# Kernel optimization log

Measured on AMD Instinct MI355X. Metric: run time of the kernel, lower is better.

## Reference

```python
import jax, jax.numpy as jnp
import numpy as np

B, C, H, W, O = 8, 128, 256, 256, 128


def setup_inputs() -> dict:
    key = jax.random.key(0)
    k1, k2, k3, k4 = jax.random.split(key, 4)
    x = jax.random.normal(k1, (B, C, H, W), dtype=jnp.float32)
    theta_s = jax.random.uniform(k2, (C, 2), dtype=jnp.float32, minval=-1.0, maxval=1.0)
    w_dw = jax.random.normal(k3, (C,), dtype=jnp.float32) * 0.1   # depthwise 1x1, groups=C
    w_pw = jax.random.normal(k4, (O, C), dtype=jnp.float32) * (1.0 / np.sqrt(C))  # pointwise 1x1
    return {"x": x, "theta_s": theta_s, "w_dw": w_dw, "w_pw": w_pw}


def reference(x, theta_s, w_dw, w_pw):
    b, c, h, w = x.shape
    # zero pad by 1 (ZeroPad2d(1)); shift operates on the padded map, output is interior
    xp = jnp.pad(x, ((0, 0), (0, 0), (1, 1), (1, 1)))
    hp, wp = h + 2, w + 2
    t = -theta_s                      # (C, 2); torch code negates theta
    ft = jnp.floor(t)
    dt = t - ft                       # fractional part, (C, 2)
    ft = ft.astype(jnp.int32)
    # interior grid of the padded map: rows/cols 1..h / 1..w
    m = jnp.arange(1, h + 1)
    n = jnp.arange(1, w + 1)
    y0 = jnp.clip(m[None, :] + ft[:, 0:1], 0, hp - 1)      # (C, h)
    y1 = jnp.clip(m[None, :] + ft[:, 0:1] + 1, 0, hp - 1)  # (C, h)
    x0 = jnp.clip(n[None, :] + ft[:, 1:2], 0, wp - 1)      # (C, w)
    x1 = jnp.clip(n[None, :] + ft[:, 1:2] + 1, 0, wp - 1)  # (C, w)
    cidx = jnp.arange(c)[:, None, None]                    # (C,1,1)
    # gather four bilinear corners for all channels at once -> (B, C, h, w)
    z1 = xp[:, cidx, y0[:, :, None], x0[:, None, :]]
    z2 = xp[:, cidx, y0[:, :, None], x1[:, None, :]]
    z3 = xp[:, cidx, y1[:, :, None], x0[:, None, :]]
    z4 = xp[:, cidx, y1[:, :, None], x1[:, None, :]]
    dy = dt[:, 0][None, :, None, None]
    dx = dt[:, 1][None, :, None, None]
    s = (z1 * (1 - dy) * (1 - dx) + z2 * (1 - dy) * dx
         + z3 * dy * (1 - dx) + z4 * dy * dx)
    # depthwise 1x1 (groups=C): per-channel scale
    s = s * w_dw[None, :, None, None]
    # pointwise 1x1
    return jnp.einsum('bchw,oc->bohw', s, w_pw)
```

## Files before the change

kernel.cpp:

```cpp
#include <hip/hip_runtime.h>

#define B_ 8
#define C_ 128
#define H_ 256
#define W_ 256
#define O_ 128
#define PAD 136
#define WT 128

typedef __bf16 bf16x4 __attribute__((ext_vector_type(4)));
typedef __bf16 bf16x8 __attribute__((ext_vector_type(8)));
typedef float floatx4 __attribute__((ext_vector_type(4)));

__device__ __forceinline__ float sfloat(float v) {
    return __int_as_float(__builtin_amdgcn_readfirstlane(__float_as_int(v)));
}

__global__ __launch_bounds__(256, 2)
void activeshift_kernel(const float* __restrict__ x,
                        const float* __restrict__ theta,
                        const float* __restrict__ wdw,
                        const float* __restrict__ wpw,
                        float* __restrict__ out)
{
    __shared__ __align__(16) __bf16 w_lds[O_ * PAD];
    __shared__ __align__(16) __bf16 s_lds[WT * PAD];
    __shared__ __align__(16) float  t_q[C_ * 4];
    __shared__ __align__(16) int    t_o[C_ * 4];

    const int bid = blockIdx.x;
    const int n   = ((bid & 7) << 9) | (bid >> 3);
    const int wt  = n & 1;
    const int h   = (n >> 1) & (H_ - 1);
    const int b   = n >> 9;
    const int w0  = wt * WT;
    const int tid = threadIdx.x;
    const int m   = h + 1;

    if (tid < C_) {
        float t0 = -theta[tid * 2 + 0];
        float t1 = -theta[tid * 2 + 1];
        float f0 = floorf(t0), f1 = floorf(t1);
        float dy = t0 - f0,    dx = t1 - f1;
        int ft0 = (int)f0, ft1 = (int)f1;
        int y0 = m + ft0, y1 = y0 + 1;
        float wy0 = (y0 >= 1 && y0 <= H_) ? 1.0f - dy : 0.0f;
        float wy1 = (y1 >= 1 && y1 <= H_) ? dy : 0.0f;
        int y0c = min(max(y0, 1), H_) - 1;
        int y1c = min(max(y1, 1), H_) - 1;
        *(floatx4*)&t_q[tid * 4] = (floatx4){wy0 * (1.0f - dx), wy0 * dx,
                                             wy1 * (1.0f - dx), wy1 * dx};
        *(int4*)&t_o[tid * 4]    = (int4){y0c * W_, y1c * W_, w0 + ft1, 0};
    }

    {
        const int c4 = (tid & 31) << 2;
        const floatx4 dv = *(const floatx4*)&wdw[c4];
        #pragma unroll
        for (int i = 0; i < 16; ++i) {
            int idx4 = tid + i * 256;
            int o    = idx4 >> 5;
            floatx4 v = *(const floatx4*)&wpw[idx4 << 2];
            bf16x4 pk = { (__bf16)(v.x * dv.x), (__bf16)(v.y * dv.y),
                          (__bf16)(v.z * dv.z), (__bf16)(v.w * dv.w) };
            *(bf16x4*)&w_lds[o * PAD + c4] = pk;
        }
    }
    __syncthreads();

    const int p     = tid & (WT - 1);
    const int halfs = __builtin_amdgcn_readfirstlane(tid >> 7);
    const size_t HW = (size_t)H_ * W_;
    const float* xb = x + (size_t)b * C_ * HW;

    for (int it = 0; it < 8; ++it) {
        const int c0 = it * 16 + halfs * 8;
        union { bf16x8 v; __bf16 e[8]; } pk;
        #pragma unroll
        for (int cc = 0; cc < 8; ++cc) {
            const int c = c0 + cc;
            const floatx4 q = *(const floatx4*)&t_q[c * 4];
            const int4   ov = *(const int4*)&t_o[c * 4];
            const float q00 = sfloat(q.x), q01 = sfloat(q.y);
            const float q10 = sfloat(q.z), q11 = sfloat(q.w);
            const int y0off = __builtin_amdgcn_readfirstlane(ov.x);
            const int y1off = __builtin_amdgcn_readfirstlane(ov.y);
            const int xoff  = __builtin_amdgcn_readfirstlane(ov.z);
            const float* r0 = xb + (size_t)c * HW + y0off;
            const float* r1 = xb + (size_t)c * HW + y1off;

            const int ix0 = p + xoff;
            const int vo0 = min(max(ix0, 0), W_ - 1);
            const int vo1 = min(max(ix0 + 1, 0), W_ - 1);
            float v00 = r0[vo0], v01 = r0[vo1];
            float v10 = r1[vo0], v11 = r1[vo1];
            if ((unsigned)ix0       > (unsigned)(W_ - 1)) { v00 = 0.f; v10 = 0.f; }
            if ((unsigned)(ix0 + 1) > (unsigned)(W_ - 1)) { v01 = 0.f; v11 = 0.f; }

            pk.e[cc] = (__bf16)(q00 * v00 + q01 * v01 + q10 * v10 + q11 * v11);
        }
        *(bf16x8*)&s_lds[p * PAD + c0] = pk.v;
    }
    __syncthreads();

    const int wid  = tid >> 6;
    const int lane = tid & 63;
    const int wo   = (wid >> 1) * 64;
    const int wp   = (wid & 1) * 64;
    const int l15  = lane & 15;
    const int quad = lane >> 4;

    floatx4 acc[4][4];
    #pragma unroll
    for (int i = 0; i < 4; ++i)
        #pragma unroll
        for (int j = 0; j < 4; ++j)
            acc[i][j] = (floatx4){0.f, 0.f, 0.f, 0.f};

    #pragma unroll
    for (int k = 0; k < C_; k += 32) {
        bf16x8 af[4], bfr[4];
        #pragma unroll
        for (int i = 0; i < 4; ++i)
            af[i] = *(const bf16x8*)&w_lds[(wo + i * 16 + l15) * PAD + k + quad * 8];
        #pragma unroll
        for (int j = 0; j < 4; ++j)
            bfr[j] = *(const bf16x8*)&s_lds[(wp + j * 16 + l15) * PAD + k + quad * 8];
        #pragma unroll
        for (int i = 0; i < 4; ++i)
            #pragma unroll
            for (int j = 0; j < 4; ++j)
                acc[i][j] = __builtin_amdgcn_mfma_f32_16x16x32_bf16(af[i], bfr[j], acc[i][j], 0, 0, 0);
    }

    float* ob = out + (size_t)b * O_ * HW + (size_t)h * W_;
    #pragma unroll
    for (int i = 0; i < 4; ++i) {
        #pragma unroll
        for (int j = 0; j < 4; ++j) {
            int pcol  = w0 + wp + j * 16 + l15;
            int obase = wo + i * 16 + quad * 4;
            float* op = ob + (size_t)obase * HW + pcol;
            #pragma unroll
            for (int r = 0; r < 4; ++r)
                op[(size_t)r * HW] = acc[i][j][r];
        }
    }
}

extern "C" void kernel_launch(void* const* d_in, const int* in_sizes, int n_in,
                              void* d_out, int out_size, void* d_ws, size_t ws_size,
                              hipStream_t stream) {
    const float* x     = (const float*)d_in[0];
    const float* theta = (const float*)d_in[1];
    const float* wdw   = (const float*)d_in[2];
    const float* wpw   = (const float*)d_in[3];
    float* out = (float*)d_out;
    activeshift_kernel<<<dim3(B_ * H_ * (W_ / WT)), dim3(256), 0, stream>>>(x, theta, wdw, wpw, out);
}
```

Measured before the change: 516.2 us.

## Drop weight LDS staging; load pointwise weights from global in MFMA loop

Removes the per-block staging of the pointwise weight matrix (scaled by depthwise weights) into LDS. The depthwise scale is folded into the bilinear coefficients instead, and the MFMA A-fragments are read straight from global memory and converted to bf16 inside the k loop. Freeing about 34KB of LDS lets launch bounds rise to 4 blocks per CU, aiming for higher occupancy. The cost is repeated global or L2 weight reads and conversions per wave. The readfirstlane scalarization of the coefficients is also dropped.

New measurement: 517.6 us. No clear change (+0.3%).

```diff
diff --git a/kernel.cpp b/kernel.cpp
--- a/kernel.cpp
+++ b/kernel.cpp
@@ -8,22 +8,16 @@
 #define PAD 136
 #define WT 128
 
-typedef __bf16 bf16x4 __attribute__((ext_vector_type(4)));
 typedef __bf16 bf16x8 __attribute__((ext_vector_type(8)));
 typedef float floatx4 __attribute__((ext_vector_type(4)));
 
-__device__ __forceinline__ float sfloat(float v) {
-    return __int_as_float(__builtin_amdgcn_readfirstlane(__float_as_int(v)));
-}
-
-__global__ __launch_bounds__(256, 2)
+__global__ __launch_bounds__(256, 4)
 void activeshift_kernel(const float* __restrict__ x,
                         const float* __restrict__ theta,
                         const float* __restrict__ wdw,
                         const float* __restrict__ wpw,
                         float* __restrict__ out)
 {
-    __shared__ __align__(16) __bf16 w_lds[O_ * PAD];
     __shared__ __align__(16) __bf16 s_lds[WT * PAD];
     __shared__ __align__(16) float  t_q[C_ * 4];
     __shared__ __align__(16) int    t_o[C_ * 4];
@@ -44,27 +38,14 @@
         float dy = t0 - f0,    dx = t1 - f1;
         int ft0 = (int)f0, ft1 = (int)f1;
         int y0 = m + ft0, y1 = y0 + 1;
-        float wy0 = (y0 >= 1 && y0 <= H_) ? 1.0f - dy : 0.0f;
-        float wy1 = (y1 >= 1 && y1 <= H_) ? dy : 0.0f;
+        float dwv = wdw[tid];
+        float wy0 = (y0 >= 1 && y0 <= H_) ? (1.0f - dy) * dwv : 0.0f;
+        float wy1 = (y1 >= 1 && y1 <= H_) ? dy * dwv : 0.0f;
         int y0c = min(max(y0, 1), H_) - 1;
         int y1c = min(max(y1, 1), H_) - 1;
         *(floatx4*)&t_q[tid * 4] = (floatx4){wy0 * (1.0f - dx), wy0 * dx,
                                              wy1 * (1.0f - dx), wy1 * dx};
         *(int4*)&t_o[tid * 4]    = (int4){y0c * W_, y1c * W_, w0 + ft1, 0};
-    }
-
-    {
-        const int c4 = (tid & 31) << 2;
-        const floatx4 dv = *(const floatx4*)&wdw[c4];
-        #pragma unroll
-        for (int i = 0; i < 16; ++i) {
-            int idx4 = tid + i * 256;
-            int o    = idx4 >> 5;
-            floatx4 v = *(const floatx4*)&wpw[idx4 << 2];
-            bf16x4 pk = { (__bf16)(v.x * dv.x), (__bf16)(v.y * dv.y),
-                          (__bf16)(v.z * dv.z), (__bf16)(v.w * dv.w) };
-            *(bf16x4*)&w_lds[o * PAD + c4] = pk;
-        }
     }
     __syncthreads();
 
@@ -81,8 +62,6 @@
             const int c = c0 + cc;
             const floatx4 q = *(const floatx4*)&t_q[c * 4];
             const int4   ov = *(const int4*)&t_o[c * 4];
-            const float q00 = sfloat(q.x), q01 = sfloat(q.y);
-            const float q10 = sfloat(q.z), q11 = sfloat(q.w);
             const int y0off = __builtin_amdgcn_readfirstlane(ov.x);
             const int y1off = __builtin_amdgcn_readfirstlane(ov.y);
             const int xoff  = __builtin_amdgcn_readfirstlane(ov.z);
@@ -97,7 +76,7 @@
             if ((unsigned)ix0       > (unsigned)(W_ - 1)) { v00 = 0.f; v10 = 0.f; }
             if ((unsigned)(ix0 + 1) > (unsigned)(W_ - 1)) { v01 = 0.f; v11 = 0.f; }
 
-            pk.e[cc] = (__bf16)(q00 * v00 + q01 * v01 + q10 * v10 + q11 * v11);
+            pk.e[cc] = (__bf16)(q.x * v00 + q.y * v01 + q.z * v10 + q.w * v11);
         }
         *(bf16x8*)&s_lds[p * PAD + c0] = pk.v;
     }
@@ -119,18 +98,21 @@
 
     #pragma unroll
     for (int k = 0; k < C_; k += 32) {
-        bf16x8 af[4], bfr[4];
-        #pragma unroll
-        for (int i = 0; i < 4; ++i)
-            af[i] = *(const bf16x8*)&w_lds[(wo + i * 16 + l15) * PAD + k + quad * 8];
+        bf16x8 bfr[4];
         #pragma unroll
         for (int j = 0; j < 4; ++j)
             bfr[j] = *(const bf16x8*)&s_lds[(wp + j * 16 + l15) * PAD + k + quad * 8];
         #pragma unroll
-        for (int i = 0; i < 4; ++i)
+        for (int i = 0; i < 4; ++i) {
+            const float* ap = wpw + (size_t)(wo + i * 16 + l15) * C_ + k + quad * 8;
+            floatx4 a0 = *(const floatx4*)ap;
+            floatx4 a1 = *(const floatx4*)(ap + 4);
+            bf16x8 af = { (__bf16)a0.x, (__bf16)a0.y, (__bf16)a0.z, (__bf16)a0.w,
+                          (__bf16)a1.x, (__bf16)a1.y, (__bf16)a1.z, (__bf16)a1.w };
             #pragma unroll
             for (int j = 0; j < 4; ++j)
-                acc[i][j] = __builtin_amdgcn_mfma_f32_16x16x32_bf16(af[i], bfr[j], acc[i][j], 0, 0, 0);
+                acc[i][j] = __builtin_amdgcn_mfma_f32_16x16x32_bf16(af, bfr[j], acc[i][j], 0, 0, 0);
+        }
     }
 
     float* ob = out + (size_t)b * O_ * HW + (size_t)h * W_;
```
